# Kernel optimization log

Hardware: AMD Instinct MI355X
Metric: run time of the kernel (lower is better)

The kernel has to match this reference:

```python
import jax, jax.numpy as jnp
import numpy as np
from jax import lax


def _conv(x, W):
    # NCHW conv, stride 1, SAME padding (padding = kernel//2 in original)
    return lax.conv_general_dilated(x, W, (1, 1), 'SAME',
                                    dimension_numbers=('NCHW', 'OIHW', 'NCHW'))


def _cconv(zr, zi, Wr, Wi, br, bi):
    # complex conv: (zr + i*zi) * (Wr + i*Wi)
    yr = _conv(zr, Wr) - _conv(zi, Wi) + br[None, :, None, None]
    yi = _conv(zr, Wi) + _conv(zi, Wr) + bi[None, :, None, None]
    return yr, yi


def setup_inputs() -> dict:
    key = jax.random.key(0)
    B, C, H, W = 16, 128, 64, 64        # C = 128 total = 64 real + 64 imag channels
    half = C // 2                        # 64 complex channels
    kin = (C + C) // 2                   # (input+hidden)/2 complex input channels = 128
    K = 3
    ks = jax.random.split(key, 20)
    inp = {
        'x':      jax.random.normal(ks[0], (B, C, H, W), jnp.float32),
        'h_prev': jax.random.normal(ks[1], (B, C, H, W), jnp.float32),
        'c_prev': jax.random.normal(ks[2], (B, C, H, W), jnp.float32),
    }
    i = 3
    for g in ('i', 'f', 'o', 'c'):
        inp['Wr_' + g] = jax.random.normal(ks[i], (half, kin, K, K), jnp.float32) * 0.05; i += 1
        inp['Wi_' + g] = jax.random.normal(ks[i], (half, kin, K, K), jnp.float32) * 0.05; i += 1
        inp['br_' + g] = jax.random.normal(ks[i], (half,), jnp.float32) * 0.05; i += 1
        inp['bi_' + g] = jax.random.normal(ks[i], (half,), jnp.float32) * 0.05; i += 1
    return inp


def reference(x, h_prev, c_prev,
              Wr_i, Wi_i, br_i, bi_i,
              Wr_f, Wi_f, br_f, bi_f,
              Wr_o, Wi_o, br_o, bi_o,
              Wr_c, Wi_c, br_c, bi_c):
    C = x.shape[1]
    h = C // 2
    xr, xi = x[:, :h], x[:, h:]
    hr, hi = h_prev[:, :h], h_prev[:, h:]
    cr, ci = c_prev[:, :h], c_prev[:, h:]

    zr = jnp.concatenate([xr, hr], axis=1)   # real part of combined
    zi = jnp.concatenate([xi, hi], axis=1)   # imag part of combined

    # gates: complex conv then split sigmoid / tanh (applied per component)
    i_r, i_i = map(jax.nn.sigmoid, _cconv(zr, zi, Wr_i, Wi_i, br_i, bi_i))
    # f gate conv output is computed but unused in final update (original bug keeps x as f)
    o_r, o_i = map(jax.nn.sigmoid, _cconv(zr, zi, Wr_o, Wi_o, br_o, bi_o))
    ct_r, ct_i = map(jnp.tanh, _cconv(zr, zi, Wr_c, Wi_c, br_c, bi_c))

    # faithful to original: f_r/f_i taken from x, not from conv_f output
    c_new_r = xr * cr - xi * ci + i_r * ct_r - i_i * ct_i
    c_new_i = xr * ci + xi * cr + i_r * ct_i + i_i * ct_r

    t_r = jnp.tanh(c_new_r)
    t_i = jnp.tanh(c_new_i)
    h_new = jnp.concatenate([o_r * t_r - o_i * t_i, o_r * t_i + o_i * t_r], axis=1)
    c_new = jnp.concatenate([c_new_r, c_new_i], axis=1)
    return h_new, c_new
```

## Files before the change

### kernel.cpp

```cpp
#include <hip/hip_runtime.h>
#include <hip/hip_bf16.h>


typedef __attribute__((ext_vector_type(8))) short short8;
typedef __attribute__((ext_vector_type(4))) float floatx4;
typedef __attribute__((ext_vector_type(4))) float float4v;

#define MTOT   65536
#define HSIZE  8388608
#define ZP_ELEMS (16 * 66 * 66 * 256)

__device__ __forceinline__ short f2bf(float f) {
  __hip_bfloat16 h = __float2bfloat16(f);
  return *reinterpret_cast<short*>(&h);
}

__device__ __forceinline__ float bf2f(short s) {
  unsigned u = ((unsigned)(unsigned short)s) << 16;
  return __uint_as_float(u);
}

__device__ __forceinline__ void gload16(const short* g, void* lds) {
  __builtin_amdgcn_global_load_lds(
      (__attribute__((address_space(1))) void*)(g),
      (__attribute__((address_space(3))) void*)(lds), 16, 0, 0);
}

__global__ __launch_bounds__(256) void halo_zero_kernel(short* __restrict__ Zp) {
  int t = blockIdx.x * 256 + threadIdx.x;
  int s   = t & 31;
  int pix = t >> 5;
  int b = pix / 260;
  int r = pix - b * 260;
  int yp, xp;
  if (r < 66)       { yp = 0;               xp = r; }
  else if (r < 132) { yp = 65;              xp = r - 66; }
  else { int r2 = r - 132; yp = 1 + (r2 >> 1); xp = (r2 & 1) * 65; }
  short8 z;
#pragma unroll
  for (int q = 0; q < 8; ++q) z[q] = 0;
  *(short8*)(Zp + (((b * 66 + yp) * 66 + xp) * 256 + s * 8)) = z;
}

__global__ __launch_bounds__(256) void pack_z_kernel(
    const float* __restrict__ xs, const float* __restrict__ hs,
    short* __restrict__ Zp) {
  __shared__ short tile[64 * 72];
  int bid = blockIdx.x;
  int y      = bid & 63;
  int half   = (bid >> 6) & 1;
  int srcSel = (bid >> 7) & 1;
  int b      = bid >> 8;
  const float* src = srcSel ? hs : xs;
  int chBase  = half * 64;
  int cinBase = half * 128 + srcSel * 64;
  int t = threadIdx.x;
  int x4 = t & 15, chq = t >> 4;
#pragma unroll
  for (int p = 0; p < 4; ++p) {
    int ch = p * 16 + chq;
    float4v f = *(const float4v*)(src + (size_t)(b * 128 + chBase + ch) * 4096 + y * 64 + x4 * 4);
#pragma unroll
    for (int e = 0; e < 4; ++e)
      tile[(x4 * 4 + e) * 72 + ch] = f2bf(f[e]);
  }
  __syncthreads();
  int x = t >> 2, seg = t & 3;
  short8 v0 = *(const short8*)(tile + x * 72 + seg * 16);
  short8 v1 = *(const short8*)(tile + x * 72 + seg * 16 + 8);
  size_t outp = ((size_t)(b * 66 + y + 1) * 66 + x + 1) * 256 + cinBase + seg * 16;
  *(short8*)(Zp + outp)     = v0;
  *(short8*)(Zp + outp + 8) = v1;
}

__global__ __launch_bounds__(256) void pack_w_kernel(
    const float* __restrict__ Wr_i, const float* __restrict__ Wi_i,
    const float* __restrict__ Wr_o, const float* __restrict__ Wi_o,
    const float* __restrict__ Wr_c, const float* __restrict__ Wi_c,
    const float* __restrict__ br_i, const float* __restrict__ bi_i,
    const float* __restrict__ br_o, const float* __restrict__ bi_o,
    const float* __restrict__ br_c, const float* __restrict__ bi_c,
    short* __restrict__ Wp, float* __restrict__ bias) {
  int g = blockIdx.x * 256 + threadIdx.x;
  if (g >= 384 * 9 * 256) return;
  int cin = g & 255;
  int tap = (g >> 8) % 9;
  int n   = g / (256 * 9);
  int part = n >> 6, ch = n & 63;
  const float *Wr, *Wi;
  if (part < 2)      { Wr = Wr_i; Wi = Wi_i; }
  else if (part < 4) { Wr = Wr_o; Wi = Wi_o; }
  else               { Wr = Wr_c; Wi = Wi_c; }
  int im = part & 1;
  int ci = cin & 127;
  int second = cin >> 7;
  const float* src = im ? (second ? Wr : Wi) : (second ? Wi : Wr);
  float f = src[(ch * 128 + ci) * 9 + tap];
  if (!im && second) f = -f;
  Wp[(n * 9 + tap) * 256 + cin] = f2bf(f);
  if (g < 384) {
    int p2 = g >> 6, c2 = g & 63;
    const float* bs = (p2 == 0) ? br_i : (p2 == 1) ? bi_i : (p2 == 2) ? br_o
                    : (p2 == 3) ? bi_o : (p2 == 4) ? br_c : bi_c;
    bias[g] = bs[c2];
  }
}

__global__ __launch_bounds__(256, 3) void conv_gemm(
    const short* __restrict__ Z, const short* __restrict__ Wp,
    const float* __restrict__ bias, __hip_bfloat16* __restrict__ gates) {
  __shared__ short8 As[1024];
  __shared__ short8 Bs[1056];

  const int tid = threadIdx.x;
  const int wv = tid >> 6, lane = tid & 63;
  const int l15 = lane & 15, l4 = lane >> 4;
  const int m0 = blockIdx.x * 128;
  const int n0 = blockIdx.y * 128;
  const int b  = m0 >> 12;
  const int y0 = (m0 >> 6) & 63;
  const int wch = (wv & 1) * 64;
  const int r2w = wv >> 1;

  floatx4 acc[4][4];
#pragma unroll
  for (int i = 0; i < 4; ++i)
#pragma unroll
    for (int j = 0; j < 4; ++j)
#pragma unroll
      for (int r = 0; r < 4; ++r) acc[i][j][r] = 0.f;

  for (int dy = -1; dy <= 1; ++dy) {
    for (int c0 = 0; c0 < 256; c0 += 64) {
#pragma unroll
      for (int it = 0; it < 5; ++it) {
        int idx = tid + it * 256;
        if (idx < 1056) {
          int r2  = (idx >= 528) ? 1 : 0;
          int rem = idx - r2 * 528;
          int col = rem >> 3, p = rem & 7;
          int g   = p ^ (col & 7);
          int ygl = b * 66 + y0 + dy + 1 + r2;
          gload16(Z + ((size_t)(ygl * 66 + col) * 256 + c0 + g * 8),
                  (void*)(Bs + (it * 256 + wv * 64)));
        }
      }
      for (int dx = -1; dx <= 1; ++dx) {
        int tap = (dy + 1) * 3 + (dx + 1);
#pragma unroll
        for (int it = 0; it < 4; ++it) {
          int idx = tid + it * 256;
          int row = idx >> 3, p = idx & 7;
          int g   = p ^ (row & 7);
          gload16(Wp + ((size_t)((n0 + row) * 9 + tap) * 256 + c0 + g * 8),
                  (void*)(As + (it * 256 + wv * 64)));
        }
        __syncthreads();
#pragma unroll
        for (int kk = 0; kk < 2; ++kk) {
          int kg = kk * 4 + l4;
          short8 a[4], bf[4];
#pragma unroll
          for (int i = 0; i < 4; ++i) {
            int row = wch + i * 16 + l15;
            a[i] = As[row * 8 + (kg ^ (row & 7))];
          }
#pragma unroll
          for (int j = 0; j < 4; ++j) {
            int col = j * 16 + l15 + dx + 1;
            bf[j] = Bs[r2w * 528 + col * 8 + (kg ^ (col & 7))];
          }
#pragma unroll
          for (int i = 0; i < 4; ++i)
#pragma unroll
            for (int j = 0; j < 4; ++j)
              acc[i][j] = __builtin_amdgcn_mfma_f32_16x16x32_bf16(a[i], bf[j], acc[i][j], 0, 0, 0);
        }
        __syncthreads();
      }
    }
  }
#pragma unroll
  for (int i = 0; i < 4; ++i)
#pragma unroll
    for (int j = 0; j < 4; ++j)
#pragma unroll
      for (int r = 0; r < 4; ++r) {
        int ch = n0 + wch + i * 16 + l4 * 4 + r;
        int px = m0 + r2w * 64 + j * 16 + l15;
        gates[(size_t)ch * MTOT + px] = __float2bfloat16(acc[i][j][r] + bias[ch]);
      }
}

__device__ __forceinline__ float fsig(float v) { return 1.f / (1.f + __expf(-v)); }
__device__ __forceinline__ float ftanh(float v) {
  float e = __expf(2.f * v);
  return 1.f - 2.f / (e + 1.f);
}

__global__ __launch_bounds__(256) void epilogue_kernel(
    const __hip_bfloat16* __restrict__ gates,
    const float* __restrict__ x,
    const float* __restrict__ c_prev,
    float* __restrict__ out) {
  int t = blockIdx.x * 256 + threadIdx.x;
  int ch = t >> 13;
  int m  = (t & 8191) << 3;
  int b = m >> 12, sp = m & 4095;

  size_t gbase = (size_t)ch * MTOT + m;
  short8 gri = *(const short8*)((const short*)gates + gbase);
  short8 gii = *(const short8*)((const short*)gates + gbase + (size_t)64 * MTOT);
  short8 gro = *(const short8*)((const short*)gates + gbase + (size_t)128 * MTOT);
  short8 gio = *(const short8*)((const short*)gates + gbase + (size_t)192 * MTOT);
  short8 grc = *(const short8*)((const short*)gates + gbase + (size_t)256 * MTOT);
  short8 gic = *(const short8*)((const short*)gates + gbase + (size_t)320 * MTOT);

  int base = (b * 128 + ch) * 4096 + sp;
  float xr[8] __attribute__((aligned(16)));
  float xi[8] __attribute__((aligned(16)));
  float cr[8] __attribute__((aligned(16)));
  float ci[8] __attribute__((aligned(16)));
  *(float4v*)(xr)     = *(const float4v*)(x + base);
  *(float4v*)(xr + 4) = *(const float4v*)(x + base + 4);
  *(float4v*)(xi)     = *(const float4v*)(x + base + 64 * 4096);
  *(float4v*)(xi + 4) = *(const float4v*)(x + base + 64 * 4096 + 4);
  *(float4v*)(cr)     = *(const float4v*)(c_prev + base);
  *(float4v*)(cr + 4) = *(const float4v*)(c_prev + base + 4);
  *(float4v*)(ci)     = *(const float4v*)(c_prev + base + 64 * 4096);
  *(float4v*)(ci + 4) = *(const float4v*)(c_prev + base + 64 * 4096 + 4);

  float hr[8] __attribute__((aligned(16)));
  float hi[8] __attribute__((aligned(16)));
  float nr[8] __attribute__((aligned(16)));
  float ni[8] __attribute__((aligned(16)));
#pragma unroll
  for (int q = 0; q < 8; ++q) {
    float i_r = fsig(bf2f(gri[q])), i_i = fsig(bf2f(gii[q]));
    float o_r = fsig(bf2f(gro[q])), o_i = fsig(bf2f(gio[q]));
    float ct_r = ftanh(bf2f(grc[q])), ct_i = ftanh(bf2f(gic[q]));
    float cnr = xr[q] * cr[q] - xi[q] * ci[q] + i_r * ct_r - i_i * ct_i;
    float cni = xr[q] * ci[q] + xi[q] * cr[q] + i_r * ct_i + i_i * ct_r;
    float tr = ftanh(cnr), ti = ftanh(cni);
    hr[q] = o_r * tr - o_i * ti;
    hi[q] = o_r * ti + o_i * tr;
    nr[q] = cnr;
    ni[q] = cni;
  }

  *(float4v*)(out + base)                         = *(const float4v*)(hr);
  *(float4v*)(out + base + 4)                     = *(const float4v*)(hr + 4);
  *(float4v*)(out + base + 64 * 4096)             = *(const float4v*)(hi);
  *(float4v*)(out + base + 64 * 4096 + 4)         = *(const float4v*)(hi + 4);
  *(float4v*)(out + HSIZE + base)                 = *(const float4v*)(nr);
  *(float4v*)(out + HSIZE + base + 4)             = *(const float4v*)(nr + 4);
  *(float4v*)(out + HSIZE + base + 64 * 4096)     = *(const float4v*)(ni);
  *(float4v*)(out + HSIZE + base + 64 * 4096 + 4) = *(const float4v*)(ni + 4);
}

extern "C" void kernel_launch(void* const* d_in, const int* in_sizes, int n_in,
                              void* d_out, int out_size, void* d_ws, size_t ws_size,
                              hipStream_t stream) {
  const float* x = (const float*)d_in[0];
  const float* h = (const float*)d_in[1];

  char* ws = (char*)d_ws;
  short* Zp   = (short*)ws;
  short* Wp   = (short*)(ws + 35684352);
  float* bias = (float*)(ws + 37453824);
  __hip_bfloat16* gates = (__hip_bfloat16*)(ws + 37455360);

  halo_zero_kernel<<<520, 256, 0, stream>>>(Zp);
  pack_z_kernel<<<4096, 256, 0, stream>>>(x, h, Zp);
  pack_w_kernel<<<3456, 256, 0, stream>>>(
      (const float*)d_in[3], (const float*)d_in[4],
      (const float*)d_in[11], (const float*)d_in[12],
      (const float*)d_in[15], (const float*)d_in[16],
      (const float*)d_in[5], (const float*)d_in[6],
      (const float*)d_in[13], (const float*)d_in[14],
      (const float*)d_in[17], (const float*)d_in[18],
      Wp, bias);
  conv_gemm<<<dim3(512, 3), 256, 0, stream>>>(Zp, Wp, bias, gates);
  epilogue_kernel<<<2048, 256, 0, stream>>>(
      gates, (const float*)d_in[0], (const float*)d_in[2],
      (float*)d_out);
}
```

Baseline: 324.9 us.

## Double-buffer LDS tiles in conv GEMM with software-pipelined async loads

Restructures the implicit-GEMM conv main loop into a fully unrolled, double-buffered pipeline. The next A (weight) and B (activation) tiles are issued via global_load_lds while the current tile is multiplied, with vmcnt waits and explicit barriers. The zero halo columns in LDS are written once instead of being loaded from the padded buffer each time, and compute runs at raised wave priority. LDS use doubles, so occupancy drops from 3 to 2 blocks per CU, and the hand-counted vmcnt waits make the schedule easy to get wrong.

```diff
diff --git a/kernel.cpp b/kernel.cpp
--- a/kernel.cpp
+++ b/kernel.cpp
@@ -8,7 +8,6 @@
 
 #define MTOT   65536
 #define HSIZE  8388608
-#define ZP_ELEMS (16 * 66 * 66 * 256)
 
 __device__ __forceinline__ short f2bf(float f) {
   __hip_bfloat16 h = __float2bfloat16(f);
@@ -106,11 +105,74 @@
   }
 }
 
-__global__ __launch_bounds__(256, 3) void conv_gemm(
+__device__ __forceinline__ void issueA(const short* __restrict__ Wp, int n0,
+                                       int ta, int dxa, short8* dst, int tid, int wv) {
+  int dy  = ta >> 2;
+  int c0  = (ta & 3) * 64;
+  int tap = dy * 3 + dxa;
+#pragma unroll
+  for (int it = 0; it < 4; ++it) {
+    int idx = tid + it * 256;
+    int row = idx >> 3, p = idx & 7;
+    int g = p ^ (row & 7);
+    gload16(Wp + ((size_t)((n0 + row) * 9 + tap) * 256 + c0 + g * 8),
+            (void*)(dst + (it * 256 + wv * 64)));
+  }
+}
+
+__device__ __forceinline__ void issueB(const short* __restrict__ Z, int zrow0,
+                                       int tb, short8* dst, int tid, int wv) {
+  int dy = tb >> 2;
+  int c0 = (tb & 3) * 64;
+#pragma unroll
+  for (int it = 0; it < 4; ++it) {
+    int idx = tid + it * 256;
+    int r2  = idx >> 9;
+    int rem = idx & 511;
+    int col = (rem >> 3) + 1;
+    int p   = rem & 7;
+    int g   = p ^ (col & 7);
+    int ygl = zrow0 + dy + r2;
+    int idx0 = it * 256 + wv * 64;
+    int r2d  = idx0 >> 9;
+    int rem0 = idx0 & 511;
+    gload16(Z + ((size_t)(ygl * 66 + col) * 256 + c0 + g * 8),
+            (void*)(dst + (r2d * 528 + 8 + rem0)));
+  }
+}
+
+template<int DXI>
+__device__ __forceinline__ void compute_step(const short8* __restrict__ Ac,
+                                             const short8* __restrict__ Bc,
+                                             floatx4 (&acc)[4][4],
+                                             int wch, int r2w, int l15, int l4) {
+#pragma unroll
+  for (int kk = 0; kk < 2; ++kk) {
+    int kg = kk * 4 + l4;
+    short8 a[4], bv[4];
+#pragma unroll
+    for (int i = 0; i < 4; ++i) {
+      int row = wch + i * 16 + l15;
+      a[i] = Ac[row * 8 + (kg ^ (row & 7))];
+    }
+#pragma unroll
+    for (int j = 0; j < 4; ++j) {
+      int col = j * 16 + l15 + DXI;
+      bv[j] = Bc[r2w * 528 + col * 8 + (kg ^ (col & 7))];
+    }
+#pragma unroll
+    for (int i = 0; i < 4; ++i)
+#pragma unroll
+      for (int j = 0; j < 4; ++j)
+        acc[i][j] = __builtin_amdgcn_mfma_f32_16x16x32_bf16(a[i], bv[j], acc[i][j], 0, 0, 0);
+  }
+}
+
+__global__ __launch_bounds__(256, 2) void conv_gemm(
     const short* __restrict__ Z, const short* __restrict__ Wp,
     const float* __restrict__ bias, __hip_bfloat16* __restrict__ gates) {
-  __shared__ short8 As[1024];
-  __shared__ short8 Bs[1056];
+  __shared__ short8 As[2][1024];
+  __shared__ short8 Bs[2][1056];
 
   const int tid = threadIdx.x;
   const int wv = tid >> 6, lane = tid & 63;
@@ -119,6 +181,7 @@
   const int n0 = blockIdx.y * 128;
   const int b  = m0 >> 12;
   const int y0 = (m0 >> 6) & 63;
+  const int zrow0 = b * 66 + y0;
   const int wch = (wv & 1) * 64;
   const int r2w = wv >> 1;
 
@@ -130,56 +193,51 @@
 #pragma unroll
       for (int r = 0; r < 4; ++r) acc[i][j][r] = 0.f;
 
-  for (int dy = -1; dy <= 1; ++dy) {
-    for (int c0 = 0; c0 < 256; c0 += 64) {
-#pragma unroll
-      for (int it = 0; it < 5; ++it) {
-        int idx = tid + it * 256;
-        if (idx < 1056) {
-          int r2  = (idx >= 528) ? 1 : 0;
-          int rem = idx - r2 * 528;
-          int col = rem >> 3, p = rem & 7;
-          int g   = p ^ (col & 7);
-          int ygl = b * 66 + y0 + dy + 1 + r2;
-          gload16(Z + ((size_t)(ygl * 66 + col) * 256 + c0 + g * 8),
-                  (void*)(Bs + (it * 256 + wv * 64)));
-        }
-      }
-      for (int dx = -1; dx <= 1; ++dx) {
-        int tap = (dy + 1) * 3 + (dx + 1);
-#pragma unroll
-        for (int it = 0; it < 4; ++it) {
-          int idx = tid + it * 256;
-          int row = idx >> 3, p = idx & 7;
-          int g   = p ^ (row & 7);
-          gload16(Wp + ((size_t)((n0 + row) * 9 + tap) * 256 + c0 + g * 8),
-                  (void*)(As + (it * 256 + wv * 64)));
-        }
-        __syncthreads();
-#pragma unroll
-        for (int kk = 0; kk < 2; ++kk) {
-          int kg = kk * 4 + l4;
-          short8 a[4], bf[4];
-#pragma unroll
-          for (int i = 0; i < 4; ++i) {
-            int row = wch + i * 16 + l15;
-            a[i] = As[row * 8 + (kg ^ (row & 7))];
-          }
-#pragma unroll
-          for (int j = 0; j < 4; ++j) {
-            int col = j * 16 + l15 + dx + 1;
-            bf[j] = Bs[r2w * 528 + col * 8 + (kg ^ (col & 7))];
-          }
-#pragma unroll
-          for (int i = 0; i < 4; ++i)
-#pragma unroll
-            for (int j = 0; j < 4; ++j)
-              acc[i][j] = __builtin_amdgcn_mfma_f32_16x16x32_bf16(a[i], bf[j], acc[i][j], 0, 0, 0);
-        }
-        __syncthreads();
-      }
-    }
-  }
+  if (tid < 64) {
+    int buf = tid >> 5, w = tid & 31;
+    int r2 = w >> 4, hi = (w >> 3) & 1, p = w & 7;
+    short8 z;
+#pragma unroll
+    for (int q = 0; q < 8; ++q) z[q] = 0;
+    Bs[buf][r2 * 528 + (hi ? 520 : 0) + p] = z;
+  }
+  issueA(Wp, n0, 0, 0, &As[0][0], tid, wv);
+  issueB(Z, zrow0, 0, &Bs[0][0], tid, wv);
+  asm volatile("s_waitcnt lgkmcnt(0)" ::: "memory");
+
+#define CONV_STEP(NW, DXI, DOA, TA, DXA, ADST, DOB, TB, BDST, AC, BC)          \
+  do {                                                                         \
+    if (DOA) issueA(Wp, n0, (TA), (DXA), &As[ADST][0], tid, wv);               \
+    if (DOB) issueB(Z, zrow0, (TB), &Bs[BDST][0], tid, wv);                    \
+    asm volatile("s_waitcnt vmcnt(" #NW ")" ::: "memory");                     \
+    __builtin_amdgcn_sched_barrier(0);                                         \
+    __builtin_amdgcn_s_barrier();                                              \
+    __builtin_amdgcn_sched_barrier(0);                                         \
+    __builtin_amdgcn_s_setprio(1);                                             \
+    compute_step<DXI>(&As[AC][0], &Bs[BC][0], acc, wch, r2w, l15, l4);         \
+    __builtin_amdgcn_s_setprio(0);                                             \
+    __builtin_amdgcn_sched_barrier(0);                                         \
+    __builtin_amdgcn_s_barrier();                                              \
+    __builtin_amdgcn_sched_barrier(0);                                         \
+  } while (0)
+
+  for (int tt = 0; tt < 5; ++tt) {
+    int t0 = tt * 2;
+    CONV_STEP(8, 0, true, t0,     1, 1, true,  t0 + 1, 1, 0, 0);
+    CONV_STEP(8, 1, true, t0,     2, 0, false, 0,      0, 1, 0);
+    CONV_STEP(4, 2, true, t0 + 1, 0, 1, false, 0,      0, 0, 0);
+    CONV_STEP(8, 0, true, t0 + 1, 1, 0, true,  t0 + 2, 0, 1, 1);
+    CONV_STEP(8, 1, true, t0 + 1, 2, 1, false, 0,      0, 0, 1);
+    CONV_STEP(4, 2, true, t0 + 2, 0, 0, false, 0,      0, 1, 1);
+  }
+  CONV_STEP(8, 0, true, 10, 1, 1, true,  11, 1, 0, 0);
+  CONV_STEP(8, 1, true, 10, 2, 0, false, 0,  0, 1, 0);
+  CONV_STEP(4, 2, true, 11, 0, 1, false, 0,  0, 0, 0);
+  CONV_STEP(4, 0, true, 11, 1, 0, false, 0,  0, 1, 1);
+  CONV_STEP(4, 1, true, 11, 2, 1, false, 0,  0, 0, 1);
+  CONV_STEP(0, 2, false, 0, 0, 0, false, 0,  0, 1, 1);
+#undef CONV_STEP
+
 #pragma unroll
   for (int i = 0; i < 4; ++i)
 #pragma unroll
```

Measured after the change: 318.2 us. -2.1%, faster.
